# Kernel optimization log

Hardware: AMD Instinct MI355X
Metric: run time of the kernel (lower is better)

Reference implementation:

```python
import jax, jax.numpy as jnp
import numpy as np

B, N, D, H, T, NHOP = 128, 256, 512, 512, 8, 1
NEG = -1e18


def _attn_score(feat, query, v, w):
    # feat: [B, Ns, H], query: [B, Nq, H] -> score [B, Nq, Ns]
    s = jnp.tanh(feat[:, None, :, :] + jnp.matmul(query, w)[:, :, None, :])
    return jnp.einsum('bqnh,h->bqn', s, v)


def _lstm(x, h0, c0, w_ih, w_hh, b_ih, b_hh):
    # x: [B, L, D]; torch nn.LSTM gate order i, f, g, o
    def step(carry, xt):
        h, c = carry
        g = xt @ w_ih.T + h @ w_hh.T + b_ih + b_hh
        i, f, gg, o = jnp.split(g, 4, axis=-1)
        c = jax.nn.sigmoid(f) * c + jax.nn.sigmoid(i) * jnp.tanh(gg)
        h = jax.nn.sigmoid(o) * jnp.tanh(c)
        return (h, c), h
    _, hs = jax.lax.scan(step, (h0, c0), jnp.swapaxes(x, 0, 1))
    return jnp.swapaxes(hs, 0, 1)  # [B, L, H]


def setup_inputs():
    key = jax.random.key(0)
    ks = jax.random.split(key, 17)
    INI = 0.01
    return {
        'attn_mem': jax.random.normal(ks[0], (B, N, D), jnp.float32),
        'lstm_in': jax.random.normal(ks[1], (B, T, D), jnp.float32),
        'mem_sizes': jax.random.randint(ks[2], (B,), 1, N + 1).astype(jnp.int32),
        'init_h': jax.random.uniform(ks[3], (H,), jnp.float32, -INI, INI),
        'init_c': jax.random.uniform(ks[4], (H,), jnp.float32, -INI, INI),
        'init_i': jax.random.uniform(ks[5], (D,), jnp.float32, -0.1, 0.1),
        'stop': jax.random.uniform(ks[6], (D,), jnp.float32, -INI, INI),
        'w_ih': jax.random.normal(ks[7], (4 * H, D), jnp.float32) * 0.02,
        'w_hh': jax.random.normal(ks[8], (4 * H, H), jnp.float32) * 0.02,
        'b_ih': jnp.zeros((4 * H,), jnp.float32),
        'b_hh': jnp.zeros((4 * H,), jnp.float32),
        'attn_wm': jax.random.normal(ks[9], (D, H), jnp.float32) * 0.02,
        'attn_wq': jax.random.normal(ks[10], (H, H), jnp.float32) * 0.02,
        'attn_v': jax.random.uniform(ks[11], (H,), jnp.float32, -INI, INI),
        'hop_wm': jax.random.normal(ks[12], (D, H), jnp.float32) * 0.02,
        'hop_wq': jax.random.normal(ks[13], (H, H), jnp.float32) * 0.02,
        'hop_v': jax.random.uniform(ks[14], (H,), jnp.float32, -INI, INI),
    }


def reference(attn_mem, lstm_in, mem_sizes, init_h, init_c, init_i, stop,
              w_ih, w_hh, b_ih, b_hh, attn_wm, attn_wq, attn_v,
              hop_wm, hop_wq, hop_v):
    b = attn_mem.shape[0]
    # append stop slot: zeros row, scatter-add stop vector at index mem_sizes[i]
    mem = jnp.concatenate([attn_mem, jnp.zeros((b, 1, D), attn_mem.dtype)], axis=1)
    mem = mem.at[jnp.arange(b), mem_sizes].add(stop)
    sizes = mem_sizes + 1
    # _prepare
    attn_feat = mem @ attn_wm   # [B, N+1, H]
    hop_feat = mem @ hop_wm     # [B, N+1, H]
    x = jnp.concatenate([jnp.broadcast_to(init_i, (b, 1, D)), lstm_in], axis=1)
    h0 = jnp.broadcast_to(init_h, (b, H))
    c0 = jnp.broadcast_to(init_c, (b, H))
    query = _lstm(x, h0, c0, w_ih, w_hh, b_ih, b_hh)  # [B, T+1, H]
    # n_hop masked glimpse attention
    mask = jnp.arange(N + 1)[None, :] < sizes[:, None]  # [B, N+1]
    for _ in range(NHOP):
        score = _attn_score(hop_feat, query, hop_v, hop_wq)
        score = jnp.where(mask[:, None, :], score, NEG)
        query = jnp.einsum('bqn,bnh->bqh', jax.nn.softmax(score, axis=-1), hop_feat)
    # final unmasked pointer scores [B, T+1, N+1]
    return _attn_score(attn_feat, query, attn_v, attn_wq)
```

## Files before the change

### kernel.cpp

```cpp
#include <hip/hip_runtime.h>
#include <hip/hip_bf16.h>
#include <math.h>

#define BB   128
#define NPTS 256
#define NP1  257
#define DD   512
#define HH   512
#define G4   2048
#define TP1  9
#define NEGF -1e18f
#define MTOT (BB * NP1)
#define CSC  2.8853900817779268f
#define L2E  1.4426950408889634f

typedef __attribute__((ext_vector_type(8))) short bf16x8;
typedef __attribute__((ext_vector_type(8))) unsigned short u16x8;
typedef __attribute__((ext_vector_type(4))) float f32x4;

__device__ __forceinline__ float bf2f(unsigned short u)
{
    union { unsigned int i; float f; } x;
    x.i = (unsigned int)u << 16;
    return x.f;
}

__device__ __forceinline__ float sigm(float x)
{
    return __builtin_amdgcn_rcpf(1.0f + __builtin_amdgcn_exp2f(-x * L2E));
}

__device__ __forceinline__ float fast_tanh(float x)
{
    float e = __builtin_amdgcn_exp2f(x * CSC);
    return 1.0f - 2.0f * __builtin_amdgcn_rcpf(e + 1.0f);
}

__device__ __forceinline__ void gl_lds16(const __hip_bfloat16* g, __hip_bfloat16* l)
{
    __builtin_amdgcn_global_load_lds(
        (const __attribute__((address_space(1))) void*)g,
        (__attribute__((address_space(3))) void*)l, 16, 0, 0);
}

__device__ __forceinline__ void stage8(const __hip_bfloat16* const* aptr,
                                       const __hip_bfloat16* const* bptr,
                                       const int* ldsoff,
                                       __hip_bfloat16* A_, __hip_bfloat16* B_, int kt)
{
#pragma unroll
    for (int s = 0; s < 4; ++s) gl_lds16(aptr[s] + kt, A_ + ldsoff[s]);
#pragma unroll
    for (int s = 0; s < 4; ++s) gl_lds16(bptr[s] + kt, B_ + ldsoff[s]);
}

__device__ __forceinline__ void gemm_step(const __hip_bfloat16* A_,
                                          const __hip_bfloat16* B_,
                                          f32x4 (&acc)[4][4],
                                          int wr, int wc, int rA, int kgrp)
{
#pragma unroll
    for (int ks = 0; ks < 2; ++ks) {
        bf16x8 af[4], bfr[4];
#pragma unroll
        for (int fi = 0; fi < 4; ++fi) {
            const int r = wr + fi * 16 + rA;
            const int ch = (ks * 4 + kgrp) ^ (r & 7);
            af[fi] = *(const bf16x8*)(A_ + r * 64 + ch * 8);
        }
#pragma unroll
        for (int fj = 0; fj < 4; ++fj) {
            const int r = wc + fj * 16 + rA;
            const int ch = (ks * 4 + kgrp) ^ (r & 7);
            bfr[fj] = *(const bf16x8*)(B_ + r * 64 + ch * 8);
        }
#pragma unroll
        for (int fi = 0; fi < 4; ++fi)
#pragma unroll
            for (int fj = 0; fj < 4; ++fj)
                acc[fi][fj] = __builtin_amdgcn_mfma_f32_16x16x32_bf16(
                    af[fi], bfr[fj], acc[fi][fj], 0, 0, 0);
    }
}

#define PIPE_ITER(I, NW, Acur, Bcur, Anxt, Bnxt)                              \
    if ((I) < 7) stage8(aptr, bptr, ldsoff, Anxt, Bnxt, ((I) + 1) * 64);      \
    asm volatile("s_waitcnt vmcnt(" NW ")" ::: "memory");                     \
    __builtin_amdgcn_s_barrier();                                             \
    asm volatile("" ::: "memory");                                            \
    gemm_step(Acur, Bcur, acc, wr, wc, rA, kgrp);                             \
    __builtin_amdgcn_s_barrier();                                             \
    asm volatile("" ::: "memory");

#define PIPE_RUN()                                                            \
    stage8(aptr, bptr, ldsoff, As0, Bs0, 0);                                  \
    PIPE_ITER(0, "8", As0, Bs0, As1, Bs1)                                     \
    PIPE_ITER(1, "8", As1, Bs1, As0, Bs0)                                     \
    PIPE_ITER(2, "8", As0, Bs0, As1, Bs1)                                     \
    PIPE_ITER(3, "8", As1, Bs1, As0, Bs0)                                     \
    PIPE_ITER(4, "8", As0, Bs0, As1, Bs1)                                     \
    PIPE_ITER(5, "8", As1, Bs1, As0, Bs0)                                     \
    PIPE_ITER(6, "8", As0, Bs0, As1, Bs1)                                     \
    PIPE_ITER(7, "0", As1, Bs1, As0, Bs0)

__global__ __launch_bounds__(256)
void k_prep(const float* __restrict__ hop_wm, const float* __restrict__ attn_wm,
            const float* __restrict__ hop_wq, const float* __restrict__ attn_wq,
            const float* __restrict__ w_ih, const float* __restrict__ w_hh,
            const float* __restrict__ b_ih, const float* __restrict__ b_hh,
            const float* __restrict__ stop, const float* __restrict__ lstm_in,
            const float* __restrict__ init_i, const float* __restrict__ init_h,
            const float* __restrict__ init_c, const float* __restrict__ Amem,
            __hip_bfloat16* __restrict__ Wt2, __hip_bfloat16* __restrict__ WqtH,
            __hip_bfloat16* __restrict__ WqtA, __hip_bfloat16* __restrict__ wih_bf,
            __hip_bfloat16* __restrict__ whh_bf, float* __restrict__ bsum,
            float* __restrict__ stopm2, __hip_bfloat16* __restrict__ Xbf,
            __hip_bfloat16* __restrict__ h_a, float* __restrict__ cbuf,
            __hip_bfloat16* __restrict__ Abf)
{
    const int x = blockIdx.x, t = threadIdx.x;
    if (x < 256) {
        __shared__ float S[64][69];
        const int mat  = x >> 6;
        const int tile = x & 63;
        const int tr = tile >> 3, tc = tile & 7;
        const float* W = (mat == 0) ? hop_wm : (mat == 1) ? attn_wm
                       : (mat == 2) ? hop_wq : attn_wq;
        __hip_bfloat16* O = (mat == 0) ? Wt2 : (mat == 1) ? (Wt2 + (size_t)512 * DD)
                          : (mat == 2) ? WqtH : WqtA;
        const float scale = (mat == 3) ? 1.0f : CSC;
#pragma unroll
        for (int k = 0; k < 4; ++k) {
            const int r = (t >> 4) + k * 16;
            const int c4 = (t & 15) * 4;
            const float4 v = *(const float4*)(W + (size_t)(tr * 64 + r) * 512 + tc * 64 + c4);
            S[r][c4] = v.x; S[r][c4 + 1] = v.y; S[r][c4 + 2] = v.z; S[r][c4 + 3] = v.w;
        }
        __syncthreads();
        const int oc = tc * 64 + (t >> 2);
        const int j0 = (t & 3) * 16;
        __hip_bfloat16 tmp[16];
#pragma unroll
        for (int j = 0; j < 16; ++j)
            tmp[j] = __float2bfloat16(scale * S[j0 + j][t >> 2]);
        *(bf16x8*)(O + (size_t)oc * 512 + tr * 64 + j0)     = *(bf16x8*)&tmp[0];
        *(bf16x8*)(O + (size_t)oc * 512 + tr * 64 + j0 + 8) = *(bf16x8*)&tmp[8];
    } else if (x == 256) {
#pragma unroll
        for (int i = 0; i < 8; ++i) {
            const int idx = t + 256 * i;
            bsum[idx] = b_ih[idx] + b_hh[idx];
        }
    } else if (x < 261) {
        const int h = (x - 257) * 256 + t;
        const float* W = (h < 512) ? hop_wm : attn_wm;
        const int col = h & 511;
        float a = 0.f;
        for (int k = 0; k < DD; ++k) a += stop[k] * W[(size_t)k * HH + col];
        stopm2[h] = CSC * a;
    } else if (x < 1413) {
        const int m = x - 261;
        const int bb = m / TP1, tt = m - bb * TP1;
        const float* src = (tt == 0) ? init_i : (lstm_in + (size_t)(bb * 8 + tt - 1) * DD);
        float2 vv = *(const float2*)(src + 2 * t);
        __hip_bfloat16* o = Xbf + (size_t)m * DD + 2 * t;
        o[0] = __float2bfloat16(vv.x);
        o[1] = __float2bfloat16(vv.y);
    } else if (x < 1669) {
        const int idx = (x - 1413) * 256 + t;
        h_a[idx]  = __float2bfloat16(init_h[idx & (HH - 1)]);
        cbuf[idx] = init_c[idx & (HH - 1)];
    } else if (x < 3717) {
        const size_t r = (size_t)(x - 1669) * DD;
        wih_bf[r + t]       = __float2bfloat16(w_ih[r + t]);
        wih_bf[r + t + 256] = __float2bfloat16(w_ih[r + t + 256]);
    } else if (x < 5765) {
        const size_t r = (size_t)(x - 3717) * DD;
        whh_bf[r + t]       = __float2bfloat16(w_hh[r + t]);
        whh_bf[r + t + 256] = __float2bfloat16(w_hh[r + t + 256]);
    } else {
        const int m = (x - 5765) * 2 + (t >> 7);
        const int b = m / NP1;
        const int n = m - b * NP1;
        const int c4 = (t & 127) * 4;
        float4 v = make_float4(0.f, 0.f, 0.f, 0.f);
        if (n < NPTS)
            v = *(const float4*)(Amem + ((size_t)(b * NPTS + n)) * DD + c4);
        __hip_bfloat16* o = Abf + (size_t)m * DD + c4;
        o[0] = __float2bfloat16(v.x);
        o[1] = __float2bfloat16(v.y);
        o[2] = __float2bfloat16(v.z);
        o[3] = __float2bfloat16(v.w);
    }
}

__global__ __launch_bounds__(256)
void k_feat2(const __hip_bfloat16* __restrict__ A,
             const __hip_bfloat16* __restrict__ Bt,
             const float* __restrict__ stopm2,
             const int* __restrict__ msz,
             __hip_bfloat16* __restrict__ E2)
{
    const int orig = blockIdx.x;
    const int wgid = (orig & 7) * 257 + (orig >> 3);
    const int m0 = (wgid >> 3) * 128;
    const int n0 = (wgid & 7) * 128;

    __shared__ __align__(16) __hip_bfloat16 SM[4][128 * 64];
    __hip_bfloat16* As0 = SM[0];
    __hip_bfloat16* Bs0 = SM[1];
    __hip_bfloat16* As1 = SM[2];
    __hip_bfloat16* Bs1 = SM[3];
    const int tid  = threadIdx.x;
    const int lane = tid & 63;
    const int wid  = tid >> 6;
    const int wr = (wid >> 1) * 64;
    const int wc = (wid & 1) * 64;

    const __hip_bfloat16* aptr[4];
    const __hip_bfloat16* bptr[4];
    int ldsoff[4];
#pragma unroll
    for (int s = 0; s < 4; ++s) {
        const int si = wid * 4 + s;
        const int o = si * 1024 + lane * 16;
        const int row = o >> 7;
        const int chunk = (o >> 4) & 7;
        const int sch = chunk ^ (row & 7);
        aptr[s] = A + (size_t)(m0 + row) * DD + sch * 8;
        bptr[s] = Bt + (size_t)(n0 + row) * DD + sch * 8;
        ldsoff[s] = si * 512;
    }

    f32x4 acc[4][4];
#pragma unroll
    for (int i = 0; i < 4; ++i)
#pragma unroll
        for (int j = 0; j < 4; ++j) acc[i][j] = (f32x4){0.f, 0.f, 0.f, 0.f};

    const int rA = lane & 15;
    const int kgrp = lane >> 4;

    PIPE_RUN()

#pragma unroll
    for (int fi = 0; fi < 4; ++fi) {
#pragma unroll
        for (int r = 0; r < 4; ++r) {
            const int m = m0 + wr + fi * 16 + (lane >> 4) * 4 + r;
            const int b = m / NP1;
            const int n = m - b * NP1;
            const bool addstop = (n == msz[b]);
#pragma unroll
            for (int fj = 0; fj < 4; ++fj) {
                const int h = n0 + wc + fj * 16 + (lane & 15);
                float v = acc[fi][fj][r];
                if (addstop) v += stopm2[h];
                E2[(size_t)m * 1024 + h] = __float2bfloat16(__builtin_amdgcn_exp2f(v));
            }
        }
    }
}

__global__ __launch_bounds__(256)
void k_gemm_bt(const __hip_bfloat16* __restrict__ A,
               const __hip_bfloat16* __restrict__ Bt,
               const float* __restrict__ bias,
               float* __restrict__ C, int ldc, int expout)
{
    __shared__ __align__(16) __hip_bfloat16 SM[4][128 * 64];
    __hip_bfloat16* As0 = SM[0];
    __hip_bfloat16* Bs0 = SM[1];
    __hip_bfloat16* As1 = SM[2];
    __hip_bfloat16* Bs1 = SM[3];
    const int tid  = threadIdx.x;
    const int lane = tid & 63;
    const int wid  = tid >> 6;
    const int m0 = blockIdx.x * 128;
    const int n0 = blockIdx.y * 128;
    const int wr = (wid >> 1) * 64;
    const int wc = (wid & 1) * 64;

    const __hip_bfloat16* aptr[4];
    const __hip_bfloat16* bptr[4];
    int ldsoff[4];
#pragma unroll
    for (int s = 0; s < 4; ++s) {
        const int si = wid * 4 + s;
        const int o = si * 1024 + lane * 16;
        const int row = o >> 7;
        const int chunk = (o >> 4) & 7;
        const int sch = chunk ^ (row & 7);
        aptr[s] = A + (size_t)(m0 + row) * DD + sch * 8;
        bptr[s] = Bt + (size_t)(n0 + row) * DD + sch * 8;
        ldsoff[s] = si * 512;
    }

    f32x4 acc[4][4];
#pragma unroll
    for (int i = 0; i < 4; ++i)
#pragma unroll
        for (int j = 0; j < 4; ++j) acc[i][j] = (f32x4){0.f, 0.f, 0.f, 0.f};

    const int rA = lane & 15;
    const int kgrp = lane >> 4;

    PIPE_RUN()

#pragma unroll
    for (int fi = 0; fi < 4; ++fi) {
#pragma unroll
        for (int r = 0; r < 4; ++r) {
            const int m = m0 + wr + fi * 16 + (lane >> 4) * 4 + r;
#pragma unroll
            for (int fj = 0; fj < 4; ++fj) {
                const int h = n0 + wc + fj * 16 + (lane & 15);
                float v = acc[fi][fj][r];
                if (bias) v += bias[h];
                if (expout) v = __builtin_amdgcn_exp2f(v);
                C[(size_t)m * ldc + h] = v;
            }
        }
    }
}

__global__ __launch_bounds__(256)
void k_lstm2(const __hip_bfloat16* __restrict__ hin,
             const __hip_bfloat16* __restrict__ whh,
             const float* __restrict__ gx,
             float* __restrict__ cbuf,
             __hip_bfloat16* __restrict__ hout,
             __hip_bfloat16* __restrict__ query,
             int t)
{
    __shared__ __align__(16) __hip_bfloat16 As[64 * 512];
    __shared__ __align__(16) __hip_bfloat16 Bs[32 * 512];
    __shared__ float Gs[64][36];
    const int tid  = threadIdx.x;
    const int lane = tid & 63;
    const int wid  = tid >> 6;
    const int m0  = blockIdx.x * 64;
    const int hc0 = blockIdx.y * 8;
    const int wy = wid >> 1, wx = wid & 1;

#pragma unroll
    for (int i = 0; i < 16; ++i) {
        const int o = (i * 256 + tid) * 16;
        const int c = o >> 13;
        const int oc = o & 8191;
        const int row = oc >> 7;
        const int ch = (oc >> 4) & 7;
        const int sch = ch ^ (row & 7);
        gl_lds16(hin + (size_t)(m0 + row) * HH + c * 64 + sch * 8, As + (o >> 1));
    }
#pragma unroll
    for (int i = 0; i < 8; ++i) {
        const int o = (i * 256 + tid) * 16;
        const int c = o >> 12;
        const int oc = o & 4095;
        const int row = oc >> 7;
        const int ch = (oc >> 4) & 7;
        const int sch = ch ^ (row & 7);
        const int brow = (row >> 3) * 512 + hc0 + (row & 7);
        gl_lds16(whh + (size_t)brow * HH + c * 64 + sch * 8, Bs + (o >> 1));
    }
    __syncthreads();

    f32x4 acc[2];
    acc[0] = (f32x4){0.f, 0.f, 0.f, 0.f};
    acc[1] = (f32x4){0.f, 0.f, 0.f, 0.f};
    const int rr = lane & 15;
    const int kg = lane >> 4;

#pragma unroll
    for (int ks = 0; ks < 16; ++ks) {
        const int c = ks >> 1, sub = ks & 1;
        const __hip_bfloat16* Ab = As + c * 4096;
        const __hip_bfloat16* Bb = Bs + c * 2048;
        const int rb = wx * 16 + rr;
        const bf16x8 bfr = *(const bf16x8*)(Bb + rb * 64 + (((sub * 4 + kg) ^ (rb & 7)) * 8));
#pragma unroll
        for (int fi = 0; fi < 2; ++fi) {
            const int ra = wy * 32 + fi * 16 + rr;
            const bf16x8 af = *(const bf16x8*)(Ab + ra * 64 + (((sub * 4 + kg) ^ (ra & 7)) * 8));
            acc[fi] = __builtin_amdgcn_mfma_f32_16x16x32_bf16(af, bfr, acc[fi], 0, 0, 0);
        }
    }

#pragma unroll
    for (int fi = 0; fi < 2; ++fi)
#pragma unroll
        for (int r = 0; r < 4; ++r)
            Gs[wy * 32 + fi * 16 + (lane >> 4) * 4 + r][wx * 16 + (lane & 15)] = acc[fi][r];
    __syncthreads();

    const int j  = tid & 7;
    const int mg = tid >> 3;
#pragma unroll
    for (int mi = 0; mi < 2; ++mi) {
        const int m = mg * 2 + mi;
        const float* gxr = gx + ((size_t)(m0 + m) * TP1 + t) * G4 + hc0 + j;
        float iv = sigm(Gs[m][j]      + gxr[0]);
        float fv = sigm(Gs[m][8 + j]  + gxr[512]);
        float gv = fast_tanh(Gs[m][16 + j] + gxr[1024]);
        float ov = sigm(Gs[m][24 + j] + gxr[1536]);
        const int ci = (m0 + m) * HH + hc0 + j;
        float cv = fv * cbuf[ci] + iv * gv;
        float hv = ov * fast_tanh(cv);
        cbuf[ci] = cv;
        hout[ci] = __float2bfloat16(hv);
        query[((size_t)(m0 + m) * TP1 + t) * HH + hc0 + j] = __float2bfloat16(hv);
    }
}

__global__ __launch_bounds__(256)
void k_score(const __hip_bfloat16* __restrict__ E2, int efoff,
             const float* __restrict__ Eq,
             const float* __restrict__ v, const int* __restrict__ msz,
             float* __restrict__ score, int masked)
{
    const int wid  = threadIdx.x >> 6;
    const int lane = threadIdx.x & 63;
    const int n = blockIdx.x * 4 + wid;
    const int b = blockIdx.y;
    if (n >= NP1) return;
    float* sp = score + (size_t)b * TP1 * NP1 + n;
    if (masked && n > msz[b]) {
        if (lane == 0)
#pragma unroll
            for (int q = 0; q < TP1; ++q) sp[q * NP1] = NEGF;
        return;
    }
    const u16x8 fu = *(const u16x8*)((const unsigned short*)E2
                                     + ((size_t)b * NP1 + n) * 1024 + efoff + lane * 8);
    float ef[8];
#pragma unroll
    for (int i = 0; i < 8; ++i) ef[i] = bf2f(fu[i]);
    const float4* v4 = (const float4*)v;
    const float4 va = v4[lane * 2], vb = v4[lane * 2 + 1];
    const float vs8 = va.x + va.y + va.z + va.w + vb.x + vb.y + vb.z + vb.w;
    float v2[8] = {2.f*va.x, 2.f*va.y, 2.f*va.z, 2.f*va.w,
                   2.f*vb.x, 2.f*vb.y, 2.f*vb.z, 2.f*vb.w};
    for (int q = 0; q < TP1; ++q) {
        const float4* q4 = (const float4*)(Eq + ((size_t)b * TP1 + q) * HH);
        const float4 qa = q4[lane * 2], qb = q4[lane * 2 + 1];
        float eq[8] = {qa.x, qa.y, qa.z, qa.w, qb.x, qb.y, qb.z, qb.w};
        float acc = 0.f;
#pragma unroll
        for (int i = 0; i < 8; ++i)
            acc = fmaf(v2[i], __builtin_amdgcn_rcpf(fmaf(ef[i], eq[i], 1.0f)), acc);
        float s = vs8 - acc;
#pragma unroll
        for (int off = 32; off; off >>= 1) s += __shfl_down(s, off);
        if (lane == 0) sp[q * NP1] = s;
    }
}

__global__ __launch_bounds__(256)
void k_softpv(const float* __restrict__ score, const __hip_bfloat16* __restrict__ E2,
              const int* __restrict__ msz, __hip_bfloat16* __restrict__ outq)
{
    const int b   = blockIdx.x;
    const int ch  = blockIdx.y;
    const int tid = threadIdx.x;
    const int lane = tid & 63, wid = tid >> 6;
    __shared__ float p[TP1][NP1 + 3];
    __shared__ float comb[TP1][256];
    const int nlim = msz[b] + 1;

    const float* sb = score + (size_t)b * TP1 * NP1;
    for (int q = wid; q < TP1; q += 4) {
        const float* srow = sb + q * NP1;
        float mx = NEGF;
        for (int n = lane; n < nlim; n += 64) mx = fmaxf(mx, srow[n]);
#pragma unroll
        for (int off = 32; off; off >>= 1) mx = fmaxf(mx, __shfl_xor(mx, off));
        float sum = 0.f;
        for (int n = lane; n < nlim; n += 64) {
            float e = __builtin_amdgcn_exp2f((srow[n] - mx) * L2E);
            p[q][n] = e;
            sum += e;
        }
#pragma unroll
        for (int off = 32; off; off >>= 1) sum += __shfl_xor(sum, off);
        float inv = 1.f / sum;
        for (int n = lane; n < nlim; n += 64) p[q][n] *= inv;
    }
    __syncthreads();

    const int ng = tid >> 7;
    const int tc = tid & 127;
    const int col = ch * 256 + tc * 2;
    const unsigned short* fb = (const unsigned short*)E2 + (size_t)b * NP1 * 1024 + col;
    float a0[TP1] = {}, a1[TP1] = {};
    for (int n = ng; n < nlim; n += 2) {
        const unsigned int u = *(const unsigned int*)(fb + (size_t)n * 1024);
        const float f0 = __builtin_amdgcn_logf(bf2f((unsigned short)(u & 0xffffu)));
        const float f1 = __builtin_amdgcn_logf(bf2f((unsigned short)(u >> 16)));
#pragma unroll
        for (int q = 0; q < TP1; ++q) {
            const float pq = p[q][n];
            a0[q] += pq * f0;
            a1[q] += pq * f1;
        }
    }
    if (ng == 1) {
#pragma unroll
        for (int q = 0; q < TP1; ++q) {
            comb[q][tc * 2]     = a0[q];
            comb[q][tc * 2 + 1] = a1[q];
        }
    }
    __syncthreads();
    if (ng == 0) {
        __hip_bfloat16* oq = outq + (size_t)(b * TP1) * HH + col;
#pragma unroll
        for (int q = 0; q < TP1; ++q) {
            oq[(size_t)q * HH]     = __float2bfloat16(a0[q] + comb[q][tc * 2]);
            oq[(size_t)q * HH + 1] = __float2bfloat16(a1[q] + comb[q][tc * 2 + 1]);
        }
    }
}

extern "C" void kernel_launch(void* const* d_in, const int* in_sizes, int n_in,
                              void* d_out, int out_size, void* d_ws, size_t ws_size,
                              hipStream_t stream)
{
    const float* attn_mem  = (const float*)d_in[0];
    const float* lstm_in   = (const float*)d_in[1];
    const int*   mem_sizes = (const int*)d_in[2];
    const float* init_h    = (const float*)d_in[3];
    const float* init_c    = (const float*)d_in[4];
    const float* init_i    = (const float*)d_in[5];
    const float* stop      = (const float*)d_in[6];
    const float* w_ih      = (const float*)d_in[7];
    const float* w_hh      = (const float*)d_in[8];
    const float* b_ih      = (const float*)d_in[9];
    const float* b_hh      = (const float*)d_in[10];
    const float* attn_wm   = (const float*)d_in[11];
    const float* attn_wq   = (const float*)d_in[12];
    const float* attn_v    = (const float*)d_in[13];
    const float* hop_wm    = (const float*)d_in[14];
    const float* hop_wq    = (const float*)d_in[15];
    const float* hop_v     = (const float*)d_in[16];
    float* out = (float*)d_out;

    char* w = (char*)d_ws;
    __hip_bfloat16* Abf    = (__hip_bfloat16*)w;  w += (size_t)MTOT * DD * 2;
    __hip_bfloat16* E2     = (__hip_bfloat16*)w;  w += (size_t)MTOT * 1024 * 2;
    __hip_bfloat16* Xbf    = (__hip_bfloat16*)w;  w += (size_t)BB * TP1 * DD * 2;
    __hip_bfloat16* Wt2    = (__hip_bfloat16*)w;  w += (size_t)1024 * DD * 2;
    __hip_bfloat16* WqtH   = (__hip_bfloat16*)w;  w += (size_t)HH * HH * 2;
    __hip_bfloat16* WqtA   = (__hip_bfloat16*)w;  w += (size_t)HH * HH * 2;
    __hip_bfloat16* wih_bf = (__hip_bfloat16*)w;  w += (size_t)G4 * DD * 2;
    __hip_bfloat16* whh_bf = (__hip_bfloat16*)w;  w += (size_t)G4 * HH * 2;
    __hip_bfloat16* h_a    = (__hip_bfloat16*)w;  w += (size_t)BB * HH * 2;
    __hip_bfloat16* h_b    = (__hip_bfloat16*)w;  w += (size_t)BB * HH * 2;
    __hip_bfloat16* query  = (__hip_bfloat16*)w;  w += (size_t)BB * TP1 * HH * 2;
    __hip_bfloat16* query2 = (__hip_bfloat16*)w;  w += (size_t)BB * TP1 * HH * 2;
    float* gatesx  = (float*)w;  w += (size_t)BB * TP1 * G4 * 4;
    float* eq      = (float*)w;  w += (size_t)BB * TP1 * HH * 4;
    float* score   = (float*)w;  w += (size_t)BB * TP1 * NP1 * 4;
    float* cbuf    = (float*)w;  w += (size_t)BB * HH * 4;
    float* stopm2  = (float*)w;  w += 1024 * 4;
    float* bsum    = (float*)w;  w += G4 * 4;

    k_prep<<<dim3(22213), dim3(256), 0, stream>>>(
        hop_wm, attn_wm, hop_wq, attn_wq, w_ih, w_hh, b_ih, b_hh,
        stop, lstm_in, init_i, init_h, init_c, attn_mem,
        Wt2, WqtH, WqtA, wih_bf, whh_bf, bsum, stopm2, Xbf, h_a, cbuf, Abf);

    k_feat2<<<dim3(2056), dim3(256), 0, stream>>>(Abf, Wt2, stopm2, mem_sizes, E2);

    k_gemm_bt<<<dim3(9, 16), dim3(256), 0, stream>>>(Xbf, wih_bf, bsum, gatesx, G4, 0);
    for (int t = 0; t < TP1; ++t) {
        const __hip_bfloat16* hin = (t & 1) ? h_b : h_a;
        __hip_bfloat16*      hout = (t & 1) ? h_a : h_b;
        k_lstm2<<<dim3(2, 64), dim3(256), 0, stream>>>(hin, whh_bf, gatesx, cbuf, hout, query, t);
    }

    k_gemm_bt<<<dim3(9, 4), dim3(256), 0, stream>>>(query, WqtH, nullptr, eq, HH, 1);
    k_score<<<dim3(65, 128), dim3(256), 0, stream>>>(E2, 0, eq, hop_v, mem_sizes, score, 1);
    k_softpv<<<dim3(128, 2), dim3(256), 0, stream>>>(score, E2, mem_sizes, query2);

    k_gemm_bt<<<dim3(9, 4), dim3(256), 0, stream>>>(query2, WqtA, nullptr, eq, HH, 1);
    k_score<<<dim3(65, 128), dim3(256), 0, stream>>>(E2, 512, eq, attn_v, mem_sizes, out, 0);
}
```

Before: 264.6 us.

## Fuse LSTM timesteps into one persistent kernel with grid barrier

Replaces nine per-timestep LSTM kernel launches with a single persistent kernel of 128 blocks that loops over timesteps and synchronises through a global atomic grid barrier. The W_hh slice stays resident in LDS across steps instead of being reloaded each launch. A second change in the score kernel pairs reciprocals, computing two terms with one rcp to cut transcendental ops. The barrier relies on all 128 blocks being co-resident and on global memory visibility of h between steps. The paired rcp may lose a little precision or overflow for large products.

```diff
diff --git a/kernel.cpp b/kernel.cpp
--- a/kernel.cpp
+++ b/kernel.cpp
@@ -13,6 +13,7 @@
 #define MTOT (BB * NP1)
 #define CSC  2.8853900817779268f
 #define L2E  1.4426950408889634f
+#define NBLSTM 128
 
 typedef __attribute__((ext_vector_type(8))) short bf16x8;
 typedef __attribute__((ext_vector_type(8))) unsigned short u16x8;
@@ -41,6 +42,23 @@
     __builtin_amdgcn_global_load_lds(
         (const __attribute__((address_space(1))) void*)g,
         (__attribute__((address_space(3))) void*)l, 16, 0, 0);
+}
+
+__device__ __forceinline__ void gridbar(int* bar, int nb)
+{
+    __syncthreads();
+    if (threadIdx.x == 0) {
+        __threadfence();
+        int g = __hip_atomic_load(bar + 1, __ATOMIC_RELAXED, __HIP_MEMORY_SCOPE_AGENT);
+        int a = __hip_atomic_fetch_add(bar, 1, __ATOMIC_ACQ_REL, __HIP_MEMORY_SCOPE_AGENT);
+        if (a == nb - 1) {
+            __hip_atomic_store(bar, 0, __ATOMIC_RELAXED, __HIP_MEMORY_SCOPE_AGENT);
+            __hip_atomic_fetch_add(bar + 1, 1, __ATOMIC_ACQ_REL, __HIP_MEMORY_SCOPE_AGENT);
+        } else {
+            while (__hip_atomic_load(bar + 1, __ATOMIC_ACQUIRE, __HIP_MEMORY_SCOPE_AGENT) == g) {}
+        }
+    }
+    __syncthreads();
 }
 
 __device__ __forceinline__ void stage8(const __hip_bfloat16* const* aptr,
@@ -116,7 +134,7 @@
             __hip_bfloat16* __restrict__ whh_bf, float* __restrict__ bsum,
             float* __restrict__ stopm2, __hip_bfloat16* __restrict__ Xbf,
             __hip_bfloat16* __restrict__ h_a, float* __restrict__ cbuf,
-            __hip_bfloat16* __restrict__ Abf)
+            __hip_bfloat16* __restrict__ Abf, int* __restrict__ bar)
 {
     const int x = blockIdx.x, t = threadIdx.x;
     if (x < 256) {
@@ -146,6 +164,7 @@
         *(bf16x8*)(O + (size_t)oc * 512 + tr * 64 + j0)     = *(bf16x8*)&tmp[0];
         *(bf16x8*)(O + (size_t)oc * 512 + tr * 64 + j0 + 8) = *(bf16x8*)&tmp[8];
     } else if (x == 256) {
+        if (t < 2) bar[t] = 0;
 #pragma unroll
         for (int i = 0; i < 8; ++i) {
             const int idx = t + 256 * i;
@@ -325,13 +344,13 @@
 }
 
 __global__ __launch_bounds__(256)
-void k_lstm2(const __hip_bfloat16* __restrict__ hin,
-             const __hip_bfloat16* __restrict__ whh,
+void k_lstm9(const __hip_bfloat16* __restrict__ whh,
              const float* __restrict__ gx,
              float* __restrict__ cbuf,
-             __hip_bfloat16* __restrict__ hout,
+             __hip_bfloat16* __restrict__ h_a,
+             __hip_bfloat16* __restrict__ h_b,
              __hip_bfloat16* __restrict__ query,
-             int t)
+             int* __restrict__ bar)
 {
     __shared__ __align__(16) __hip_bfloat16 As[64 * 512];
     __shared__ __align__(16) __hip_bfloat16 Bs[32 * 512];
@@ -342,17 +361,9 @@
     const int m0  = blockIdx.x * 64;
     const int hc0 = blockIdx.y * 8;
     const int wy = wid >> 1, wx = wid & 1;
-
-#pragma unroll
-    for (int i = 0; i < 16; ++i) {
-        const int o = (i * 256 + tid) * 16;
-        const int c = o >> 13;
-        const int oc = o & 8191;
-        const int row = oc >> 7;
-        const int ch = (oc >> 4) & 7;
-        const int sch = ch ^ (row & 7);
-        gl_lds16(hin + (size_t)(m0 + row) * HH + c * 64 + sch * 8, As + (o >> 1));
-    }
+    const int rr = lane & 15;
+    const int kg = lane >> 4;
+
 #pragma unroll
     for (int i = 0; i < 8; ++i) {
         const int o = (i * 256 + tid) * 16;
@@ -364,52 +375,67 @@
         const int brow = (row >> 3) * 512 + hc0 + (row & 7);
         gl_lds16(whh + (size_t)brow * HH + c * 64 + sch * 8, Bs + (o >> 1));
     }
-    __syncthreads();
-
-    f32x4 acc[2];
-    acc[0] = (f32x4){0.f, 0.f, 0.f, 0.f};
-    acc[1] = (f32x4){0.f, 0.f, 0.f, 0.f};
-    const int rr = lane & 15;
-    const int kg = lane >> 4;
-
-#pragma unroll
-    for (int ks = 0; ks < 16; ++ks) {
-        const int c = ks >> 1, sub = ks & 1;
-        const __hip_bfloat16* Ab = As + c * 4096;
-        const __hip_bfloat16* Bb = Bs + c * 2048;
-        const int rb = wx * 16 + rr;
-        const bf16x8 bfr = *(const bf16x8*)(Bb + rb * 64 + (((sub * 4 + kg) ^ (rb & 7)) * 8));
-#pragma unroll
-        for (int fi = 0; fi < 2; ++fi) {
-            const int ra = wy * 32 + fi * 16 + rr;
-            const bf16x8 af = *(const bf16x8*)(Ab + ra * 64 + (((sub * 4 + kg) ^ (ra & 7)) * 8));
-            acc[fi] = __builtin_amdgcn_mfma_f32_16x16x32_bf16(af, bfr, acc[fi], 0, 0, 0);
-        }
-    }
-
-#pragma unroll
-    for (int fi = 0; fi < 2; ++fi)
-#pragma unroll
-        for (int r = 0; r < 4; ++r)
-            Gs[wy * 32 + fi * 16 + (lane >> 4) * 4 + r][wx * 16 + (lane & 15)] = acc[fi][r];
-    __syncthreads();
-
-    const int j  = tid & 7;
-    const int mg = tid >> 3;
-#pragma unroll
-    for (int mi = 0; mi < 2; ++mi) {
-        const int m = mg * 2 + mi;
-        const float* gxr = gx + ((size_t)(m0 + m) * TP1 + t) * G4 + hc0 + j;
-        float iv = sigm(Gs[m][j]      + gxr[0]);
-        float fv = sigm(Gs[m][8 + j]  + gxr[512]);
-        float gv = fast_tanh(Gs[m][16 + j] + gxr[1024]);
-        float ov = sigm(Gs[m][24 + j] + gxr[1536]);
-        const int ci = (m0 + m) * HH + hc0 + j;
-        float cv = fv * cbuf[ci] + iv * gv;
-        float hv = ov * fast_tanh(cv);
-        cbuf[ci] = cv;
-        hout[ci] = __float2bfloat16(hv);
-        query[((size_t)(m0 + m) * TP1 + t) * HH + hc0 + j] = __float2bfloat16(hv);
+
+    for (int t = 0; t < TP1; ++t) {
+        const __hip_bfloat16* hin = (t & 1) ? h_b : h_a;
+        __hip_bfloat16*      hout = (t & 1) ? h_a : h_b;
+
+#pragma unroll
+        for (int i = 0; i < 16; ++i) {
+            const int o = (i * 256 + tid) * 16;
+            const int c = o >> 13;
+            const int oc = o & 8191;
+            const int row = oc >> 7;
+            const int ch = (oc >> 4) & 7;
+            const int sch = ch ^ (row & 7);
+            gl_lds16(hin + (size_t)(m0 + row) * HH + c * 64 + sch * 8, As + (o >> 1));
+        }
+        __syncthreads();
+
+        f32x4 acc[2];
+        acc[0] = (f32x4){0.f, 0.f, 0.f, 0.f};
+        acc[1] = (f32x4){0.f, 0.f, 0.f, 0.f};
+#pragma unroll
+        for (int ks = 0; ks < 16; ++ks) {
+            const int c = ks >> 1, sub = ks & 1;
+            const __hip_bfloat16* Ab = As + c * 4096;
+            const __hip_bfloat16* Bb = Bs + c * 2048;
+            const int rb = wx * 16 + rr;
+            const bf16x8 bfr = *(const bf16x8*)(Bb + rb * 64 + (((sub * 4 + kg) ^ (rb & 7)) * 8));
+#pragma unroll
+            for (int fi = 0; fi < 2; ++fi) {
+                const int ra = wy * 32 + fi * 16 + rr;
+                const bf16x8 af = *(const bf16x8*)(Ab + ra * 64 + (((sub * 4 + kg) ^ (ra & 7)) * 8));
+                acc[fi] = __builtin_amdgcn_mfma_f32_16x16x32_bf16(af, bfr, acc[fi], 0, 0, 0);
+            }
+        }
+
+#pragma unroll
+        for (int fi = 0; fi < 2; ++fi)
+#pragma unroll
+            for (int r = 0; r < 4; ++r)
+                Gs[wy * 32 + fi * 16 + (lane >> 4) * 4 + r][wx * 16 + (lane & 15)] = acc[fi][r];
+        __syncthreads();
+
+        const int j  = tid & 7;
+        const int mg = tid >> 3;
+#pragma unroll
+        for (int mi = 0; mi < 2; ++mi) {
+            const int m = mg * 2 + mi;
+            const float* gxr = gx + ((size_t)(m0 + m) * TP1 + t) * G4 + hc0 + j;
+            float iv = sigm(Gs[m][j]      + gxr[0]);
+            float fv = sigm(Gs[m][8 + j]  + gxr[512]);
+            float gv = fast_tanh(Gs[m][16 + j] + gxr[1024]);
+            float ov = sigm(Gs[m][24 + j] + gxr[1536]);
+            const int ci = (m0 + m) * HH + hc0 + j;
+            float cv = fv * cbuf[ci] + iv * gv;
+            float hv = ov * fast_tanh(cv);
+            cbuf[ci] = cv;
+            hout[ci] = __float2bfloat16(hv);
+            query[((size_t)(m0 + m) * TP1 + t) * HH + hc0 + j] = __float2bfloat16(hv);
+        }
+
+        if (t < TP1 - 1) gridbar(bar, NBLSTM);
     }
 }
 
@@ -447,8 +473,12 @@
         float eq[8] = {qa.x, qa.y, qa.z, qa.w, qb.x, qb.y, qb.z, qb.w};
         float acc = 0.f;
 #pragma unroll
-        for (int i = 0; i < 8; ++i)
-            acc = fmaf(v2[i], __builtin_amdgcn_rcpf(fmaf(ef[i], eq[i], 1.0f)), acc);
+        for (int i = 0; i < 8; i += 2) {
+            const float x0 = fmaf(ef[i],     eq[i],     1.0f);
+            const float x1 = fmaf(ef[i + 1], eq[i + 1], 1.0f);
+            const float num = fmaf(v2[i], x1, v2[i + 1] * x0);
+            acc = fmaf(num, __builtin_amdgcn_rcpf(x0 * x1), acc);
+        }
         float s = vs8 - acc;
 #pragma unroll
         for (int off = 32; off; off >>= 1) s += __shfl_down(s, off);
@@ -564,20 +594,17 @@
     float* cbuf    = (float*)w;  w += (size_t)BB * HH * 4;
     float* stopm2  = (float*)w;  w += 1024 * 4;
     float* bsum    = (float*)w;  w += G4 * 4;
+    int*   bar     = (int*)w;    w += 2 * sizeof(int);
 
     k_prep<<<dim3(22213), dim3(256), 0, stream>>>(
         hop_wm, attn_wm, hop_wq, attn_wq, w_ih, w_hh, b_ih, b_hh,
         stop, lstm_in, init_i, init_h, init_c, attn_mem,
-        Wt2, WqtH, WqtA, wih_bf, whh_bf, bsum, stopm2, Xbf, h_a, cbuf, Abf);
+        Wt2, WqtH, WqtA, wih_bf, whh_bf, bsum, stopm2, Xbf, h_a, cbuf, Abf, bar);
 
     k_feat2<<<dim3(2056), dim3(256), 0, stream>>>(Abf, Wt2, stopm2, mem_sizes, E2);
 
     k_gemm_bt<<<dim3(9, 16), dim3(256), 0, stream>>>(Xbf, wih_bf, bsum, gatesx, G4, 0);
-    for (int t = 0; t < TP1; ++t) {
-        const __hip_bfloat16* hin = (t & 1) ? h_b : h_a;
-        __hip_bfloat16*      hout = (t & 1) ? h_a : h_b;
-        k_lstm2<<<dim3(2, 64), dim3(256), 0, stream>>>(hin, whh_bf, gatesx, cbuf, hout, query, t);
-    }
+    k_lstm9<<<dim3(2, 64), dim3(256), 0, stream>>>(whh_bf, gatesx, cbuf, h_a, h_b, query, bar);
 
     k_gemm_bt<<<dim3(9, 4), dim3(256), 0, stream>>>(query, WqtH, nullptr, eq, HH, 1);
     k_score<<<dim3(65, 128), dim3(256), 0, stream>>>(E2, 0, eq, hop_v, mem_sizes, score, 1);
```

Measured after the change: 362.0 us. 36.8% more time.

## Merge LSTM input GEMM into feature GEMM launch and pair reciprocals in score

Applied to the files above, without the earlier changes.

The LSTM input-projection GEMM (Xbf x w_ih plus bias) runs as extra workgroups appended to the k_feat2 grid instead of as a separate k_gemm_bt launch. This removes a launch and lets the small GEMM fill idle CUs alongside the large feature GEMM. The score kernel also combines two reciprocals into one by using a common denominator, trading rcp instructions for a few multiplies. The combined form carries a small risk of overflow or precision loss when the product of the two denominators is large.

```diff
diff --git a/kernel.cpp b/kernel.cpp
--- a/kernel.cpp
+++ b/kernel.cpp
@@ -13,6 +13,8 @@
 #define MTOT (BB * NP1)
 #define CSC  2.8853900817779268f
 #define L2E  1.4426950408889634f
+#define NFEAT 2056
+#define NGX   144
 
 typedef __attribute__((ext_vector_type(8))) short bf16x8;
 typedef __attribute__((ext_vector_type(8))) unsigned short u16x8;
@@ -199,12 +201,28 @@
              const __hip_bfloat16* __restrict__ Bt,
              const float* __restrict__ stopm2,
              const int* __restrict__ msz,
-             __hip_bfloat16* __restrict__ E2)
+             __hip_bfloat16* __restrict__ E2,
+             const __hip_bfloat16* __restrict__ Xbf,
+             const __hip_bfloat16* __restrict__ wih,
+             const float* __restrict__ bsum,
+             float* __restrict__ gatesx)
 {
     const int orig = blockIdx.x;
-    const int wgid = (orig & 7) * 257 + (orig >> 3);
-    const int m0 = (wgid >> 3) * 128;
-    const int n0 = (wgid & 7) * 128;
+    const bool isg = (orig >= NFEAT);
+    int m0, n0;
+    const __hip_bfloat16* Ause;
+    const __hip_bfloat16* Buse;
+    if (!isg) {
+        const int wgid = (orig & 7) * 257 + (orig >> 3);
+        m0 = (wgid >> 3) * 128;
+        n0 = (wgid & 7) * 128;
+        Ause = A;  Buse = Bt;
+    } else {
+        const int idx = orig - NFEAT;
+        m0 = (idx >> 4) * 128;
+        n0 = (idx & 15) * 128;
+        Ause = Xbf;  Buse = wih;
+    }
 
     __shared__ __align__(16) __hip_bfloat16 SM[4][128 * 64];
     __hip_bfloat16* As0 = SM[0];
@@ -227,8 +245,8 @@
         const int row = o >> 7;
         const int chunk = (o >> 4) & 7;
         const int sch = chunk ^ (row & 7);
-        aptr[s] = A + (size_t)(m0 + row) * DD + sch * 8;
-        bptr[s] = Bt + (size_t)(n0 + row) * DD + sch * 8;
+        aptr[s] = Ause + (size_t)(m0 + row) * DD + sch * 8;
+        bptr[s] = Buse + (size_t)(n0 + row) * DD + sch * 8;
         ldsoff[s] = si * 512;
     }
 
@@ -243,20 +261,35 @@
 
     PIPE_RUN()
 
-#pragma unroll
-    for (int fi = 0; fi < 4; ++fi) {
-#pragma unroll
-        for (int r = 0; r < 4; ++r) {
-            const int m = m0 + wr + fi * 16 + (lane >> 4) * 4 + r;
-            const int b = m / NP1;
-            const int n = m - b * NP1;
-            const bool addstop = (n == msz[b]);
-#pragma unroll
-            for (int fj = 0; fj < 4; ++fj) {
-                const int h = n0 + wc + fj * 16 + (lane & 15);
-                float v = acc[fi][fj][r];
-                if (addstop) v += stopm2[h];
-                E2[(size_t)m * 1024 + h] = __float2bfloat16(__builtin_amdgcn_exp2f(v));
+    if (!isg) {
+#pragma unroll
+        for (int fi = 0; fi < 4; ++fi) {
+#pragma unroll
+            for (int r = 0; r < 4; ++r) {
+                const int m = m0 + wr + fi * 16 + (lane >> 4) * 4 + r;
+                const int b = m / NP1;
+                const int n = m - b * NP1;
+                const bool addstop = (n == msz[b]);
+#pragma unroll
+                for (int fj = 0; fj < 4; ++fj) {
+                    const int h = n0 + wc + fj * 16 + (lane & 15);
+                    float v = acc[fi][fj][r];
+                    if (addstop) v += stopm2[h];
+                    E2[(size_t)m * 1024 + h] = __float2bfloat16(__builtin_amdgcn_exp2f(v));
+                }
+            }
+        }
+    } else {
+#pragma unroll
+        for (int fi = 0; fi < 4; ++fi) {
+#pragma unroll
+            for (int r = 0; r < 4; ++r) {
+                const int m = m0 + wr + fi * 16 + (lane >> 4) * 4 + r;
+#pragma unroll
+                for (int fj = 0; fj < 4; ++fj) {
+                    const int h = n0 + wc + fj * 16 + (lane & 15);
+                    gatesx[(size_t)m * G4 + h] = acc[fi][fj][r] + bsum[h];
+                }
             }
         }
     }
@@ -447,8 +480,12 @@
         float eq[8] = {qa.x, qa.y, qa.z, qa.w, qb.x, qb.y, qb.z, qb.w};
         float acc = 0.f;
 #pragma unroll
-        for (int i = 0; i < 8; ++i)
-            acc = fmaf(v2[i], __builtin_amdgcn_rcpf(fmaf(ef[i], eq[i], 1.0f)), acc);
+        for (int i = 0; i < 8; i += 2) {
+            const float x0 = fmaf(ef[i],     eq[i],     1.0f);
+            const float x1 = fmaf(ef[i + 1], eq[i + 1], 1.0f);
+            const float num = fmaf(v2[i], x1, v2[i + 1] * x0);
+            acc = fmaf(num, __builtin_amdgcn_rcpf(x0 * x1), acc);
+        }
         float s = vs8 - acc;
 #pragma unroll
         for (int off = 32; off; off >>= 1) s += __shfl_down(s, off);
@@ -570,9 +607,9 @@
         stop, lstm_in, init_i, init_h, init_c, attn_mem,
         Wt2, WqtH, WqtA, wih_bf, whh_bf, bsum, stopm2, Xbf, h_a, cbuf, Abf);
 
-    k_feat2<<<dim3(2056), dim3(256), 0, stream>>>(Abf, Wt2, stopm2, mem_sizes, E2);
-
-    k_gemm_bt<<<dim3(9, 16), dim3(256), 0, stream>>>(Xbf, wih_bf, bsum, gatesx, G4, 0);
+    k_feat2<<<dim3(NFEAT + NGX), dim3(256), 0, stream>>>(
+        Abf, Wt2, stopm2, mem_sizes, E2, Xbf, wih_bf, bsum, gatesx);
+
     for (int t = 0; t < TP1; ++t) {
         const __hip_bfloat16* hin = (t & 1) ? h_b : h_a;
         __hip_bfloat16*      hout = (t & 1) ? h_a : h_b;
```

After: 249.3 us. 5.8% less time.
